# Optimization experiments

Hardware: AMD Instinct MI355X
Metric: run time of the kernel (lower is better)

## Reference

```python
import jax, jax.numpy as jnp
import numpy as np

GAMMA = 0.5
NUM_ITER = 5


def setup_inputs() -> dict:
    key = jax.random.key(0)
    k1, k2 = jax.random.split(key)
    V, L = 10242, 42
    def_idxs = jax.random.uniform(k1, (V, L), dtype=jnp.float32, minval=1e-4, maxval=1.0)
    def_cont_ico_crf = jax.random.normal(k2, (V, 3), dtype=jnp.float32)
    # learned parameters, initialized as in the module
    filter_weights = jnp.ones((V, V), dtype=jnp.float32)
    spatial_weights = 4.0 * jnp.eye(V, dtype=jnp.float32)
    comp_matrix = jnp.eye(L, dtype=jnp.float32)
    return {
        "def_idxs": def_idxs,
        "def_cont_ico_crf": def_cont_ico_crf,
        "filter_weights": filter_weights,
        "spatial_weights": spatial_weights,
        "comp_matrix": comp_matrix,
    }


def reference(def_idxs, def_cont_ico_crf, filter_weights, spatial_weights, comp_matrix):
    V = def_cont_ico_crf.shape[0]
    # pairwise squared L2 distances between control points: [V, V]
    sq = jnp.sum(def_cont_ico_crf * def_cont_ico_crf, axis=1)
    d2 = sq[:, None] + sq[None, :] - 2.0 * (def_cont_ico_crf @ def_cont_ico_crf.T)
    smooth_filter = jnp.exp(-d2 / (2.0 * GAMMA ** 2))
    idx = jnp.arange(V)
    smooth_filter = smooth_filter.at[idx, idx].set(0.0)  # fill_diagonal_(0)

    U = jnp.log(jnp.clip(def_idxs, 1e-06, 1.0))  # unary potentials [V, L]
    q = jax.nn.softmax(U, axis=1)
    filter_mat = filter_weights * smooth_filter

    for _ in range(NUM_ITER):
        phi_t = filter_mat @ q                      # message passing [V, L]
        phi = -(spatial_weights @ phi_t)            # spatial reweighting
        phi = phi @ comp_matrix                     # label compatibility
        q = jax.nn.softmax(U - phi, axis=1)
    return q
```

## Files before the change

### kernel.cpp

```cpp
#include <hip/hip_runtime.h>
#include <stdint.h>

#define Vn 10242
#define Ln 42
#define LPn 48
#define VPn 10496
#define RBn 41
#define JPAD 10368
#define NITER 5
#define SCL 1.69864360f
#define BR 128

typedef float4 f4;
typedef short bf16x8 __attribute__((ext_vector_type(8)));
typedef float f32x4 __attribute__((ext_vector_type(4)));

__device__ __forceinline__ unsigned cvtpk_bf16(float a, float b) {
    unsigned r;
    asm("v_cvt_pk_bf16_f32 %0, %1, %2" : "=v"(r) : "v"(a), "v"(b));
    return r;
}
__device__ __forceinline__ unsigned short f2bf_rne(float f) {
    unsigned u = __float_as_uint(f);
    u = (u + 0x7fffu + ((u >> 16) & 1u)) >> 16;
    return (unsigned short)u;
}
__device__ __forceinline__ float bf2f(unsigned short h) {
    return __uint_as_float(((unsigned)h) << 16);
}

__global__ __launch_bounds__(256) void k_detect(const float* __restrict__ F,
                                                const float* __restrict__ S,
                                                int* flags, float* __restrict__ diagS) {
    int jj = blockIdx.x * 256 + threadIdx.x;
    if (jj >= Vn / 2) return;
    int j = jj * 2;
    const float c0 = F[0];
    int violF = 0, violS = 0;
    for (int i = blockIdx.y; i < Vn; i += (int)gridDim.y) {
        size_t off = (size_t)i * Vn + j;
        float2 f = *(const float2*)(F + off);
        float2 s = *(const float2*)(S + off);
        violF |= (f.x != c0) | (f.y != c0);
        if (i == j)          { diagS[j] = s.x;     violS |= (s.y != 0.0f); }
        else if (i == j + 1) { diagS[j + 1] = s.y; violS |= (s.x != 0.0f); }
        else                 violS |= (s.x != 0.0f) | (s.y != 0.0f);
    }
    if (violF) atomicOr(&flags[0], 1);
    if (violS) atomicOr(&flags[1], 1);
}

__global__ void k_detC(const float* __restrict__ Cm, int* flags) {
    int viol = 0;
    for (int idx = threadIdx.x; idx < Ln * Ln; idx += 256) {
        int r = idx / Ln, c = idx - r * Ln;
        float expct = (r == c) ? 1.0f : 0.0f;
        viol |= (Cm[idx] != expct);
    }
    if (viol) atomicOr(&flags[3], 1);
}

__global__ __launch_bounds__(256) void k_initU(const float* __restrict__ didx,
                                               const float* __restrict__ coords,
                                               float* __restrict__ U, float* __restrict__ qA,
                                               float* __restrict__ qB,
                                               unsigned short* __restrict__ qTAh,
                                               unsigned short* __restrict__ qTAl,
                                               unsigned short* __restrict__ qTBh,
                                               unsigned short* __restrict__ qTBl,
                                               float* __restrict__ xyz) {
    int row = blockIdx.x * 256 + threadIdx.x;
    if (row >= Vn) {
        #pragma unroll
        for (int l = 0; l < LPn; ++l) {
            U[(size_t)row * LPn + l] = 0.0f;
            qA[(size_t)row * LPn + l] = 0.0f;
            qB[(size_t)row * LPn + l] = 0.0f;
            qTAh[(size_t)l * VPn + row] = 0;
            qTAl[(size_t)l * VPn + row] = 0;
            qTBh[(size_t)l * VPn + row] = 0;
            qTBl[(size_t)l * VPn + row] = 0;
        }
        *(f4*)(xyz + (size_t)row * 4) = make_float4(0.f, 0.f, 0.f, 0.f);
        return;
    }
    float ux = SCL * coords[(size_t)row * 3 + 0];
    float uy = SCL * coords[(size_t)row * 3 + 1];
    float uz = SCL * coords[(size_t)row * 3 + 2];
    float ss = ux * ux + uy * uy + uz * uz;
    *(f4*)(xyz + (size_t)row * 4) = make_float4(ux, uy, uz, ss);
    float u[Ln];
    float mx = -3.0e38f;
    #pragma unroll
    for (int l = 0; l < Ln; ++l) {
        float x = didx[(size_t)row * Ln + l];
        x = fminf(fmaxf(x, 1e-6f), 1.0f);
        u[l] = __logf(x);
        mx = fmaxf(mx, u[l]);
    }
    float s = 0.0f;
    float e[Ln];
    #pragma unroll
    for (int l = 0; l < Ln; ++l) { e[l] = __expf(u[l] - mx); s += e[l]; }
    float inv = 1.0f / s;
    #pragma unroll
    for (int l = 0; l < Ln; ++l) {
        float qv = e[l] * inv;
        unsigned short h = f2bf_rne(qv);
        U[(size_t)row * LPn + l] = u[l];
        qA[(size_t)row * LPn + l] = qv;
        qTAh[(size_t)l * VPn + row] = h;
        qTAl[(size_t)l * VPn + row] = f2bf_rne(qv - bf2f(h));
    }
    #pragma unroll
    for (int l = Ln; l < LPn; ++l) {
        U[(size_t)row * LPn + l] = 0.0f;
        qA[(size_t)row * LPn + l] = 0.0f;
        qB[(size_t)row * LPn + l] = 0.0f;
        qTAh[(size_t)l * VPn + row] = 0;
        qTAl[(size_t)l * VPn + row] = 0;
        qTBh[(size_t)l * VPn + row] = 0;
        qTBl[(size_t)l * VPn + row] = 0;
    }
}

__global__ __launch_bounds__(256, 3) void k_phi_f(const unsigned short* __restrict__ qTh,
                                                  const unsigned short* __restrict__ qTl,
                                                  const f4* __restrict__ xyz4,
                                                  float* __restrict__ part,
                                                  const int* __restrict__ flags, int jchunk) {
    if (flags[0]) return;
    __shared__ uint4 Ah[8][BR];
    __shared__ uint4 Al[8][BR];
    __shared__ uint4 Bh[LPn][8];
    __shared__ uint4 Bl[LPn][8];
    const int t = threadIdx.x;
    const int lane = t & 63;
    const int wv = t >> 6;
    const int lo16 = lane & 15, hi4 = lane >> 4;
    const int rowbase = blockIdx.x * BR;
    f4 p0 = xyz4[rowbase + lane];
    f4 p1 = xyz4[rowbase + lane + 64];
    const float v0x = 2.f * p0.x, v0y = 2.f * p0.y, v0z = 2.f * p0.z, ns0 = -p0.w;
    const float v1x = 2.f * p1.x, v1y = 2.f * p1.y, v1z = 2.f * p1.z, ns1 = -p1.w;
    f32x4 acc[2][3];
    #pragma unroll
    for (int rs = 0; rs < 2; ++rs)
        #pragma unroll
        for (int cs = 0; cs < 3; ++cs) acc[rs][cs] = (f32x4){0.f, 0.f, 0.f, 0.f};
    const int j0 = blockIdx.y * jchunk;
    int j1 = j0 + jchunk; if (j1 > JPAD) j1 = JPAD;
    const int n0 = t >> 3, sl0 = t & 7;
    const int s1 = t + 256;
    const int n1 = s1 >> 3, sl1 = s1 & 7;
    const bool has1 = (s1 < LPn * 8);
    for (int jt = j0; jt < j1; jt += 64) {
        uint4 bh0 = *(const uint4*)(qTh + (size_t)n0 * VPn + jt + sl0 * 8);
        uint4 bl0 = *(const uint4*)(qTl + (size_t)n0 * VPn + jt + sl0 * 8);
        uint4 bh1, bl1;
        if (has1) {
            bh1 = *(const uint4*)(qTh + (size_t)n1 * VPn + jt + sl1 * 8);
            bl1 = *(const uint4*)(qTl + (size_t)n1 * VPn + jt + sl1 * 8);
        }
        const int jb = __builtin_amdgcn_readfirstlane(jt + wv * 16);
        unsigned ph0[8], ph1[8], pl0[8], pl1[8];
        #pragma unroll
        for (int m = 0; m < 16; m += 2) {
            f4 qa = xyz4[jb + m];
            f4 qb = xyz4[jb + m + 1];
            float wa0 = exp2f(fmaf(v0z, qa.z, fmaf(v0y, qa.y, fmaf(v0x, qa.x, ns0 - qa.w))));
            float wb0 = exp2f(fmaf(v0z, qb.z, fmaf(v0y, qb.y, fmaf(v0x, qb.x, ns0 - qb.w))));
            float wa1 = exp2f(fmaf(v1z, qa.z, fmaf(v1y, qa.y, fmaf(v1x, qa.x, ns1 - qa.w))));
            float wb1 = exp2f(fmaf(v1z, qb.z, fmaf(v1y, qb.y, fmaf(v1x, qb.x, ns1 - qb.w))));
            unsigned h0 = cvtpk_bf16(wa0, wb0);
            unsigned h1 = cvtpk_bf16(wa1, wb1);
            ph0[m >> 1] = h0;
            ph1[m >> 1] = h1;
            pl0[m >> 1] = cvtpk_bf16(wa0 - __uint_as_float(h0 << 16),
                                     wb0 - __uint_as_float(h0 & 0xffff0000u));
            pl1[m >> 1] = cvtpk_bf16(wa1 - __uint_as_float(h1 << 16),
                                     wb1 - __uint_as_float(h1 & 0xffff0000u));
        }
        __syncthreads();
        Ah[2 * wv][lane]          = make_uint4(ph0[0], ph0[1], ph0[2], ph0[3]);
        Ah[2 * wv + 1][lane]      = make_uint4(ph0[4], ph0[5], ph0[6], ph0[7]);
        Ah[2 * wv][lane + 64]     = make_uint4(ph1[0], ph1[1], ph1[2], ph1[3]);
        Ah[2 * wv + 1][lane + 64] = make_uint4(ph1[4], ph1[5], ph1[6], ph1[7]);
        Al[2 * wv][lane]          = make_uint4(pl0[0], pl0[1], pl0[2], pl0[3]);
        Al[2 * wv + 1][lane]      = make_uint4(pl0[4], pl0[5], pl0[6], pl0[7]);
        Al[2 * wv][lane + 64]     = make_uint4(pl1[0], pl1[1], pl1[2], pl1[3]);
        Al[2 * wv + 1][lane + 64] = make_uint4(pl1[4], pl1[5], pl1[6], pl1[7]);
        Bh[n0][sl0 ^ (n0 & 7)] = bh0;
        Bl[n0][sl0 ^ (n0 & 7)] = bl0;
        if (has1) {
            Bh[n1][sl1 ^ (n1 & 7)] = bh1;
            Bl[n1][sl1 ^ (n1 & 7)] = bl1;
        }
        __syncthreads();
        #pragma unroll
        for (int kk = 0; kk < 2; ++kk) {
            bf16x8 a0h = *(bf16x8*)&Ah[kk * 4 + hi4][wv * 32 + lo16];
            bf16x8 a1h = *(bf16x8*)&Ah[kk * 4 + hi4][wv * 32 + 16 + lo16];
            bf16x8 a0l = *(bf16x8*)&Al[kk * 4 + hi4][wv * 32 + lo16];
            bf16x8 a1l = *(bf16x8*)&Al[kk * 4 + hi4][wv * 32 + 16 + lo16];
            #pragma unroll
            for (int cs = 0; cs < 3; ++cs) {
                int n = cs * 16 + lo16;
                int slot = (kk * 4 + hi4) ^ (n & 7);
                bf16x8 bh = *(bf16x8*)&Bh[n][slot];
                bf16x8 bl = *(bf16x8*)&Bl[n][slot];
                acc[0][cs] = __builtin_amdgcn_mfma_f32_16x16x32_bf16(a0h, bh, acc[0][cs], 0, 0, 0);
                acc[0][cs] = __builtin_amdgcn_mfma_f32_16x16x32_bf16(a0h, bl, acc[0][cs], 0, 0, 0);
                acc[0][cs] = __builtin_amdgcn_mfma_f32_16x16x32_bf16(a0l, bh, acc[0][cs], 0, 0, 0);
                acc[0][cs] = __builtin_amdgcn_mfma_f32_16x16x32_bf16(a0l, bl, acc[0][cs], 0, 0, 0);
                acc[1][cs] = __builtin_amdgcn_mfma_f32_16x16x32_bf16(a1h, bh, acc[1][cs], 0, 0, 0);
                acc[1][cs] = __builtin_amdgcn_mfma_f32_16x16x32_bf16(a1h, bl, acc[1][cs], 0, 0, 0);
                acc[1][cs] = __builtin_amdgcn_mfma_f32_16x16x32_bf16(a1l, bh, acc[1][cs], 0, 0, 0);
                acc[1][cs] = __builtin_amdgcn_mfma_f32_16x16x32_bf16(a1l, bl, acc[1][cs], 0, 0, 0);
            }
        }
    }
    size_t pb = (size_t)blockIdx.y * LPn * VPn;
    #pragma unroll
    for (int rs = 0; rs < 2; ++rs)
        #pragma unroll
        for (int cs = 0; cs < 3; ++cs) {
            int col = cs * 16 + lo16;
            int row = rowbase + wv * 32 + rs * 16 + hi4 * 4;
            *(f4*)(part + pb + (size_t)col * VPn + row) =
                make_float4(acc[rs][cs][0], acc[rs][cs][1], acc[rs][cs][2], acc[rs][cs][3]);
        }
}

template <int USEG>
__device__ __forceinline__ void mat_gen_body(const float* __restrict__ W,
                                             const float* __restrict__ X,
                                             const float* __restrict__ xyz,
                                             float* __restrict__ part, int jchunk) {
    __shared__ float ldsW[256][33];
    int t = threadIdx.x;
    int row = blockIdx.x * 256 + t;
    bool act = (row < Vn);
    int j0 = blockIdx.y * jchunk;
    int j1 = j0 + jchunk; if (j1 > Vn) j1 = Vn;
    f4 xi = make_float4(0.f, 0.f, 0.f, 0.f);
    if (USEG && act) xi = *(const f4*)(xyz + (size_t)row * 4);
    f4 acc[12];
    #pragma unroll
    for (int c = 0; c < 12; ++c) acc[c] = make_float4(0.f, 0.f, 0.f, 0.f);
    for (int jt = j0; jt < j1; jt += 32) {
        __syncthreads();
        #pragma unroll
        for (int k = 0; k < 8; ++k) {
            int idx = t + k * 256;
            int r = idx >> 3;
            int cc = (idx & 7) << 2;
            int rr = blockIdx.x * 256 + r;
            int jc = jt + cc;
            float v0 = 0.f, v1 = 0.f, v2 = 0.f, v3 = 0.f;
            if (rr < Vn) {
                const float* wp = W + (size_t)rr * Vn + jc;
                if (jc + 0 < Vn) v0 = wp[0];
                if (jc + 1 < Vn) v1 = wp[1];
                if (jc + 2 < Vn) v2 = wp[2];
                if (jc + 3 < Vn) v3 = wp[3];
            }
            ldsW[r][cc + 0] = v0; ldsW[r][cc + 1] = v1;
            ldsW[r][cc + 2] = v2; ldsW[r][cc + 3] = v3;
        }
        __syncthreads();
        int jend = j1 - jt; if (jend > 32) jend = 32;
        for (int jj = 0; jj < jend; ++jj) {
            int j = jt + jj;
            float f = ldsW[t][jj];
            if (USEG) {
                f4 xj = *(const f4*)(xyz + (size_t)j * 4);
                float dx = xi.x - xj.x, dy = xi.y - xj.y, dz = xi.z - xj.z;
                float t2 = dx * dx; t2 = fmaf(dy, dy, t2); t2 = fmaf(dz, dz, t2);
                float w = exp2f(-t2);
                w = (j == row) ? 0.0f : w;
                f *= w;
            }
            const f4* qr = (const f4*)(X + (size_t)j * LPn);
            #pragma unroll
            for (int c = 0; c < 12; ++c) {
                f4 qv = qr[c];
                acc[c].x = fmaf(f, qv.x, acc[c].x);
                acc[c].y = fmaf(f, qv.y, acc[c].y);
                acc[c].z = fmaf(f, qv.z, acc[c].z);
                acc[c].w = fmaf(f, qv.w, acc[c].w);
            }
        }
    }
    size_t base = (size_t)blockIdx.y * LPn * VPn + row;
    if (act) {
        #pragma unroll
        for (int c = 0; c < 12; ++c) {
            part[base + (size_t)(4 * c + 0) * VPn] = acc[c].x;
            part[base + (size_t)(4 * c + 1) * VPn] = acc[c].y;
            part[base + (size_t)(4 * c + 2) * VPn] = acc[c].z;
            part[base + (size_t)(4 * c + 3) * VPn] = acc[c].w;
        }
    } else if (row < VPn) {
        #pragma unroll
        for (int c = 0; c < LPn; ++c) part[base + (size_t)c * VPn] = 0.0f;
    }
}

__global__ __launch_bounds__(256) void k_phi_g(const float* __restrict__ W,
                                               const float* __restrict__ q,
                                               const float* __restrict__ xyz,
                                               float* __restrict__ part,
                                               const int* __restrict__ flags, int jchunk) {
    if (!flags[0]) return;
    mat_gen_body<1>(W, q, xyz, part, jchunk);
}

__global__ __launch_bounds__(256) void k_sp(const float* __restrict__ Sw,
                                            const float* __restrict__ phi,
                                            float* __restrict__ part,
                                            const int* __restrict__ flags, int jchunk) {
    if (!flags[1]) return;
    mat_gen_body<0>(Sw, phi, (const float*)nullptr, part, jchunk);
}

__global__ __launch_bounds__(256) void k_R0(const float* __restrict__ part,
                                            const unsigned short* __restrict__ qTh,
                                            const unsigned short* __restrict__ qTl,
                                            float* __restrict__ phi,
                                            const int* __restrict__ flags,
                                            int NS, int gate) {
    if (gate && !flags[1]) return;
    int tg = blockIdx.x * 256 + threadIdx.x;
    int c = tg / (VPn / 4);
    int r4 = (tg - c * (VPn / 4)) * 4;
    f4 s = make_float4(0.f, 0.f, 0.f, 0.f);
    for (int n = 0; n < NS; ++n) {
        f4 v = *(const f4*)(part + ((size_t)n * LPn + c) * VPn + r4);
        s.x += v.x; s.y += v.y; s.z += v.z; s.w += v.w;
    }
    if (!gate && !flags[0]) {
        ushort4 h = *(const ushort4*)(qTh + (size_t)c * VPn + r4);
        ushort4 l = *(const ushort4*)(qTl + (size_t)c * VPn + r4);
        s.x -= bf2f(h.x) + bf2f(l.x);
        s.y -= bf2f(h.y) + bf2f(l.y);
        s.z -= bf2f(h.z) + bf2f(l.z);
        s.w -= bf2f(h.w) + bf2f(l.w);
    }
    phi[(size_t)(r4 + 0) * LPn + c] = s.x;
    phi[(size_t)(r4 + 1) * LPn + c] = s.y;
    phi[(size_t)(r4 + 2) * LPn + c] = s.z;
    phi[(size_t)(r4 + 3) * LPn + c] = s.w;
}

__global__ __launch_bounds__(256) void k_B(const float* __restrict__ U,
                                           const float* __restrict__ phi,
                                           const float* __restrict__ phi2,
                                           const float* __restrict__ diagS,
                                           const float* __restrict__ Cm,
                                           const float* __restrict__ Fw,
                                           const int* __restrict__ flags,
                                           float* __restrict__ qn,
                                           unsigned short* __restrict__ qTnh,
                                           unsigned short* __restrict__ qTnl,
                                           float* __restrict__ outp, int last) {
    __shared__ float ldsC[Ln][LPn];
    int t = threadIdx.x;
    if (flags[3]) {
        for (int idx = t; idx < Ln * LPn; idx += 256) {
            int m = idx / LPn, l = idx - m * LPn;
            ldsC[m][l] = (l < Ln) ? Cm[(size_t)m * Ln + l] : 0.0f;
        }
    }
    __syncthreads();
    int row = blockIdx.x * 256 + t;
    if (row >= Vn) return;
    const float* src = flags[1] ? phi2 : phi;
    float pt[LPn];
    #pragma unroll
    for (int c = 0; c < 12; ++c) {
        f4 v = *(const f4*)(src + (size_t)row * LPn + 4 * c);
        pt[4 * c + 0] = v.x; pt[4 * c + 1] = v.y;
        pt[4 * c + 2] = v.z; pt[4 * c + 3] = v.w;
    }
    float scale = (flags[0] ? 1.0f : Fw[0]) * (flags[1] ? 1.0f : diagS[row]);
    float ph[LPn];
    if (flags[3]) {
        #pragma unroll
        for (int c = 0; c < LPn; ++c) ph[c] = 0.f;
        #pragma unroll
        for (int m = 0; m < Ln; ++m) {
            float pm = pt[m];
            #pragma unroll
            for (int c = 0; c < 12; ++c) {
                f4 cv = *(const f4*)&ldsC[m][4 * c];
                ph[4 * c + 0] = fmaf(pm, cv.x, ph[4 * c + 0]);
                ph[4 * c + 1] = fmaf(pm, cv.y, ph[4 * c + 1]);
                ph[4 * c + 2] = fmaf(pm, cv.z, ph[4 * c + 2]);
                ph[4 * c + 3] = fmaf(pm, cv.w, ph[4 * c + 3]);
            }
        }
    } else {
        #pragma unroll
        for (int c = 0; c < LPn; ++c) ph[c] = pt[c];
    }
    float lg[LPn];
    #pragma unroll
    for (int c = 0; c < 12; ++c) {
        f4 uv = *(const f4*)(U + (size_t)row * LPn + 4 * c);
        lg[4 * c + 0] = uv.x + scale * ph[4 * c + 0];
        lg[4 * c + 1] = uv.y + scale * ph[4 * c + 1];
        lg[4 * c + 2] = uv.z + scale * ph[4 * c + 2];
        lg[4 * c + 3] = uv.w + scale * ph[4 * c + 3];
    }
    float mx = lg[0];
    #pragma unroll
    for (int l = 1; l < Ln; ++l) mx = fmaxf(mx, lg[l]);
    float s = 0.f;
    float e[LPn];
    #pragma unroll
    for (int l = 0; l < Ln; ++l) { e[l] = __expf(lg[l] - mx); s += e[l]; }
    #pragma unroll
    for (int l = Ln; l < LPn; ++l) e[l] = 0.f;
    float inv = 1.0f / s;
    #pragma unroll
    for (int c = 0; c < 12; ++c) {
        f4 v = make_float4(e[4 * c + 0] * inv, e[4 * c + 1] * inv,
                           e[4 * c + 2] * inv, e[4 * c + 3] * inv);
        *(f4*)(qn + (size_t)row * LPn + 4 * c) = v;
    }
    #pragma unroll
    for (int l = 0; l < Ln; ++l) {
        float qv = e[l] * inv;
        unsigned short h = f2bf_rne(qv);
        qTnh[(size_t)l * VPn + row] = h;
        qTnl[(size_t)l * VPn + row] = f2bf_rne(qv - bf2f(h));
    }
    if (last) {
        #pragma unroll
        for (int l = 0; l < Ln; ++l) outp[(size_t)row * Ln + l] = e[l] * inv;
    }
}

extern "C" void kernel_launch(void* const* d_in, const int* in_sizes, int n_in,
                              void* d_out, int out_size, void* d_ws, size_t ws_size,
                              hipStream_t stream) {
    const float* didx   = (const float*)d_in[0];
    const float* coords = (const float*)d_in[1];
    const float* Fw     = (const float*)d_in[2];
    const float* Sw     = (const float*)d_in[3];
    const float* Cm     = (const float*)d_in[4];
    float* outp = (float*)d_out;
    float* wsf = (float*)d_ws;

    int*   flags = (int*)wsf;
    float* diagS = wsf + 16;
    float* xyz   = diagS + VPn;
    float* U     = xyz + (size_t)VPn * 4;
    float* qA    = U + (size_t)VPn * LPn;
    float* qB    = qA + (size_t)VPn * LPn;
    float* phi   = qB + (size_t)VPn * LPn;
    float* phi2  = phi + (size_t)VPn * LPn;
    unsigned short* qTAh = (unsigned short*)(phi2 + (size_t)VPn * LPn);
    unsigned short* qTAl = qTAh + (size_t)LPn * VPn;
    unsigned short* qTBh = qTAl + (size_t)LPn * VPn;
    unsigned short* qTBl = qTBh + (size_t)LPn * VPn;
    float* part  = (float*)(qTBl + (size_t)LPn * VPn);

    size_t base_f = 16 + (size_t)VPn * (1 + 4) + (size_t)VPn * LPn * 5 + (size_t)VPn * LPn * 2;
    int NS = 8;
    while (NS > 1 && (base_f + (size_t)NS * LPn * VPn) * 4 > ws_size) NS >>= 1;
    int jchunkF = ((JPAD / 64 + NS - 1) / NS) * 64;
    int jchunkG = (((Vn + NS - 1) / NS) + 31) & ~31;

    hipMemsetAsync(flags, 0, 16, stream);
    hipLaunchKernelGGL(k_detect, dim3((Vn / 2 + 255) / 256, 1024), dim3(256), 0, stream,
                       Fw, Sw, flags, diagS);
    hipLaunchKernelGGL(k_detC, dim3(1), dim3(256), 0, stream, Cm, flags);
    hipLaunchKernelGGL(k_initU, dim3(RBn), dim3(256), 0, stream,
                       didx, coords, U, qA, qB, qTAh, qTAl, qTBh, qTBl, xyz);

    float* qcur = qA;  float* qnxt = qB;
    unsigned short* qThc = qTAh;  unsigned short* qTlc = qTAl;
    unsigned short* qThn = qTBh;  unsigned short* qTln = qTBl;
    for (int it = 0; it < NITER; ++it) {
        hipLaunchKernelGGL(k_phi_f, dim3(VPn / BR, NS), dim3(256), 0, stream,
                           qThc, qTlc, (const f4*)xyz, part, flags, jchunkF);
        hipLaunchKernelGGL(k_phi_g, dim3(RBn, NS), dim3(256), 0, stream,
                           Fw, qcur, xyz, part, flags, jchunkG);
        hipLaunchKernelGGL(k_R0, dim3(LPn * (VPn / 4) / 256), dim3(256), 0, stream,
                           part, qThc, qTlc, phi, flags, NS, 0);
        hipLaunchKernelGGL(k_sp, dim3(RBn, NS), dim3(256), 0, stream,
                           Sw, phi, part, flags, jchunkG);
        hipLaunchKernelGGL(k_R0, dim3(LPn * (VPn / 4) / 256), dim3(256), 0, stream,
                           part, qThc, qTlc, phi2, flags, NS, 1);
        hipLaunchKernelGGL(k_B, dim3(RBn), dim3(256), 0, stream,
                           U, phi, phi2, diagS, Cm, Fw, flags, qnxt, qThn, qTln, outp,
                           (it == NITER - 1) ? 1 : 0);
        float* tq = qcur; qcur = qnxt; qnxt = tq;
        unsigned short* th = qThc; qThc = qThn; qThn = th;
        unsigned short* tl = qTlc; qTlc = qTln; qTln = tl;
    }
}
```

Before: 653.5 us.

## Merge phi kernels, drop low×low MFMA term, split j range nine ways

Merges the fast-path and general-path phi kernels into one launch that branches on the detection flag, with the two shared-memory layouts overlaid in a union. The split-bf16 product drops the low×low term, cutting MFMA count per tile from 24 to 18. The j-range split count starts at 9 instead of 8 and falls back one step at a time. Fewer MFMAs and one fewer launch per iteration reduce compute and dispatch overhead, at a small accuracy cost from the omitted correction term and one more partial buffer to reduce.

```diff
diff --git a/kernel.cpp b/kernel.cpp
--- a/kernel.cpp
+++ b/kernel.cpp
@@ -124,120 +124,22 @@
     }
 }
 
-__global__ __launch_bounds__(256, 3) void k_phi_f(const unsigned short* __restrict__ qTh,
-                                                  const unsigned short* __restrict__ qTl,
-                                                  const f4* __restrict__ xyz4,
-                                                  float* __restrict__ part,
-                                                  const int* __restrict__ flags, int jchunk) {
-    if (flags[0]) return;
-    __shared__ uint4 Ah[8][BR];
-    __shared__ uint4 Al[8][BR];
-    __shared__ uint4 Bh[LPn][8];
-    __shared__ uint4 Bl[LPn][8];
-    const int t = threadIdx.x;
-    const int lane = t & 63;
-    const int wv = t >> 6;
-    const int lo16 = lane & 15, hi4 = lane >> 4;
-    const int rowbase = blockIdx.x * BR;
-    f4 p0 = xyz4[rowbase + lane];
-    f4 p1 = xyz4[rowbase + lane + 64];
-    const float v0x = 2.f * p0.x, v0y = 2.f * p0.y, v0z = 2.f * p0.z, ns0 = -p0.w;
-    const float v1x = 2.f * p1.x, v1y = 2.f * p1.y, v1z = 2.f * p1.z, ns1 = -p1.w;
-    f32x4 acc[2][3];
-    #pragma unroll
-    for (int rs = 0; rs < 2; ++rs)
-        #pragma unroll
-        for (int cs = 0; cs < 3; ++cs) acc[rs][cs] = (f32x4){0.f, 0.f, 0.f, 0.f};
-    const int j0 = blockIdx.y * jchunk;
-    int j1 = j0 + jchunk; if (j1 > JPAD) j1 = JPAD;
-    const int n0 = t >> 3, sl0 = t & 7;
-    const int s1 = t + 256;
-    const int n1 = s1 >> 3, sl1 = s1 & 7;
-    const bool has1 = (s1 < LPn * 8);
-    for (int jt = j0; jt < j1; jt += 64) {
-        uint4 bh0 = *(const uint4*)(qTh + (size_t)n0 * VPn + jt + sl0 * 8);
-        uint4 bl0 = *(const uint4*)(qTl + (size_t)n0 * VPn + jt + sl0 * 8);
-        uint4 bh1, bl1;
-        if (has1) {
-            bh1 = *(const uint4*)(qTh + (size_t)n1 * VPn + jt + sl1 * 8);
-            bl1 = *(const uint4*)(qTl + (size_t)n1 * VPn + jt + sl1 * 8);
-        }
-        const int jb = __builtin_amdgcn_readfirstlane(jt + wv * 16);
-        unsigned ph0[8], ph1[8], pl0[8], pl1[8];
-        #pragma unroll
-        for (int m = 0; m < 16; m += 2) {
-            f4 qa = xyz4[jb + m];
-            f4 qb = xyz4[jb + m + 1];
-            float wa0 = exp2f(fmaf(v0z, qa.z, fmaf(v0y, qa.y, fmaf(v0x, qa.x, ns0 - qa.w))));
-            float wb0 = exp2f(fmaf(v0z, qb.z, fmaf(v0y, qb.y, fmaf(v0x, qb.x, ns0 - qb.w))));
-            float wa1 = exp2f(fmaf(v1z, qa.z, fmaf(v1y, qa.y, fmaf(v1x, qa.x, ns1 - qa.w))));
-            float wb1 = exp2f(fmaf(v1z, qb.z, fmaf(v1y, qb.y, fmaf(v1x, qb.x, ns1 - qb.w))));
-            unsigned h0 = cvtpk_bf16(wa0, wb0);
-            unsigned h1 = cvtpk_bf16(wa1, wb1);
-            ph0[m >> 1] = h0;
-            ph1[m >> 1] = h1;
-            pl0[m >> 1] = cvtpk_bf16(wa0 - __uint_as_float(h0 << 16),
-                                     wb0 - __uint_as_float(h0 & 0xffff0000u));
-            pl1[m >> 1] = cvtpk_bf16(wa1 - __uint_as_float(h1 << 16),
-                                     wb1 - __uint_as_float(h1 & 0xffff0000u));
-        }
-        __syncthreads();
-        Ah[2 * wv][lane]          = make_uint4(ph0[0], ph0[1], ph0[2], ph0[3]);
-        Ah[2 * wv + 1][lane]      = make_uint4(ph0[4], ph0[5], ph0[6], ph0[7]);
-        Ah[2 * wv][lane + 64]     = make_uint4(ph1[0], ph1[1], ph1[2], ph1[3]);
-        Ah[2 * wv + 1][lane + 64] = make_uint4(ph1[4], ph1[5], ph1[6], ph1[7]);
-        Al[2 * wv][lane]          = make_uint4(pl0[0], pl0[1], pl0[2], pl0[3]);
-        Al[2 * wv + 1][lane]      = make_uint4(pl0[4], pl0[5], pl0[6], pl0[7]);
-        Al[2 * wv][lane + 64]     = make_uint4(pl1[0], pl1[1], pl1[2], pl1[3]);
-        Al[2 * wv + 1][lane + 64] = make_uint4(pl1[4], pl1[5], pl1[6], pl1[7]);
-        Bh[n0][sl0 ^ (n0 & 7)] = bh0;
-        Bl[n0][sl0 ^ (n0 & 7)] = bl0;
-        if (has1) {
-            Bh[n1][sl1 ^ (n1 & 7)] = bh1;
-            Bl[n1][sl1 ^ (n1 & 7)] = bl1;
-        }
-        __syncthreads();
-        #pragma unroll
-        for (int kk = 0; kk < 2; ++kk) {
-            bf16x8 a0h = *(bf16x8*)&Ah[kk * 4 + hi4][wv * 32 + lo16];
-            bf16x8 a1h = *(bf16x8*)&Ah[kk * 4 + hi4][wv * 32 + 16 + lo16];
-            bf16x8 a0l = *(bf16x8*)&Al[kk * 4 + hi4][wv * 32 + lo16];
-            bf16x8 a1l = *(bf16x8*)&Al[kk * 4 + hi4][wv * 32 + 16 + lo16];
-            #pragma unroll
-            for (int cs = 0; cs < 3; ++cs) {
-                int n = cs * 16 + lo16;
-                int slot = (kk * 4 + hi4) ^ (n & 7);
-                bf16x8 bh = *(bf16x8*)&Bh[n][slot];
-                bf16x8 bl = *(bf16x8*)&Bl[n][slot];
-                acc[0][cs] = __builtin_amdgcn_mfma_f32_16x16x32_bf16(a0h, bh, acc[0][cs], 0, 0, 0);
-                acc[0][cs] = __builtin_amdgcn_mfma_f32_16x16x32_bf16(a0h, bl, acc[0][cs], 0, 0, 0);
-                acc[0][cs] = __builtin_amdgcn_mfma_f32_16x16x32_bf16(a0l, bh, acc[0][cs], 0, 0, 0);
-                acc[0][cs] = __builtin_amdgcn_mfma_f32_16x16x32_bf16(a0l, bl, acc[0][cs], 0, 0, 0);
-                acc[1][cs] = __builtin_amdgcn_mfma_f32_16x16x32_bf16(a1h, bh, acc[1][cs], 0, 0, 0);
-                acc[1][cs] = __builtin_amdgcn_mfma_f32_16x16x32_bf16(a1h, bl, acc[1][cs], 0, 0, 0);
-                acc[1][cs] = __builtin_amdgcn_mfma_f32_16x16x32_bf16(a1l, bh, acc[1][cs], 0, 0, 0);
-                acc[1][cs] = __builtin_amdgcn_mfma_f32_16x16x32_bf16(a1l, bl, acc[1][cs], 0, 0, 0);
-            }
-        }
-    }
-    size_t pb = (size_t)blockIdx.y * LPn * VPn;
-    #pragma unroll
-    for (int rs = 0; rs < 2; ++rs)
-        #pragma unroll
-        for (int cs = 0; cs < 3; ++cs) {
-            int col = cs * 16 + lo16;
-            int row = rowbase + wv * 32 + rs * 16 + hi4 * 4;
-            *(f4*)(part + pb + (size_t)col * VPn + row) =
-                make_float4(acc[rs][cs][0], acc[rs][cs][1], acc[rs][cs][2], acc[rs][cs][3]);
-        }
-}
+union ShPhi {
+    struct {
+        uint4 Ah[8][BR];
+        uint4 Al[8][BR];
+        uint4 Bh[LPn][8];
+        uint4 Bl[LPn][8];
+    } f;
+    float w[256][33];
+};
 
 template <int USEG>
 __device__ __forceinline__ void mat_gen_body(const float* __restrict__ W,
                                              const float* __restrict__ X,
                                              const float* __restrict__ xyz,
-                                             float* __restrict__ part, int jchunk) {
-    __shared__ float ldsW[256][33];
+                                             float* __restrict__ part, int jchunk,
+                                             ShPhi& sh) {
     int t = threadIdx.x;
     int row = blockIdx.x * 256 + t;
     bool act = (row < Vn);
@@ -265,14 +167,14 @@
                 if (jc + 2 < Vn) v2 = wp[2];
                 if (jc + 3 < Vn) v3 = wp[3];
             }
-            ldsW[r][cc + 0] = v0; ldsW[r][cc + 1] = v1;
-            ldsW[r][cc + 2] = v2; ldsW[r][cc + 3] = v3;
+            sh.w[r][cc + 0] = v0; sh.w[r][cc + 1] = v1;
+            sh.w[r][cc + 2] = v2; sh.w[r][cc + 3] = v3;
         }
         __syncthreads();
         int jend = j1 - jt; if (jend > 32) jend = 32;
         for (int jj = 0; jj < jend; ++jj) {
             int j = jt + jj;
-            float f = ldsW[t][jj];
+            float f = sh.w[t][jj];
             if (USEG) {
                 f4 xj = *(const f4*)(xyz + (size_t)j * 4);
                 float dx = xi.x - xj.x, dy = xi.y - xj.y, dz = xi.z - xj.z;
@@ -307,13 +209,114 @@
     }
 }
 
-__global__ __launch_bounds__(256) void k_phi_g(const float* __restrict__ W,
-                                               const float* __restrict__ q,
-                                               const float* __restrict__ xyz,
-                                               float* __restrict__ part,
-                                               const int* __restrict__ flags, int jchunk) {
-    if (!flags[0]) return;
-    mat_gen_body<1>(W, q, xyz, part, jchunk);
+__global__ __launch_bounds__(256, 3) void k_phi(const unsigned short* __restrict__ qTh,
+                                                const unsigned short* __restrict__ qTl,
+                                                const f4* __restrict__ xyz4,
+                                                const float* __restrict__ Fw,
+                                                const float* __restrict__ q,
+                                                float* __restrict__ part,
+                                                const int* __restrict__ flags,
+                                                int jchunkF, int jchunkG) {
+    __shared__ ShPhi sh;
+    if (flags[0]) {
+        if (blockIdx.x >= RBn) return;
+        mat_gen_body<1>(Fw, q, (const float*)xyz4, part, jchunkG, sh);
+        return;
+    }
+    const int t = threadIdx.x;
+    const int lane = t & 63;
+    const int wv = t >> 6;
+    const int lo16 = lane & 15, hi4 = lane >> 4;
+    const int rowbase = blockIdx.x * BR;
+    f4 p0 = xyz4[rowbase + lane];
+    f4 p1 = xyz4[rowbase + lane + 64];
+    const float v0x = 2.f * p0.x, v0y = 2.f * p0.y, v0z = 2.f * p0.z, ns0 = -p0.w;
+    const float v1x = 2.f * p1.x, v1y = 2.f * p1.y, v1z = 2.f * p1.z, ns1 = -p1.w;
+    f32x4 acc[2][3];
+    #pragma unroll
+    for (int rs = 0; rs < 2; ++rs)
+        #pragma unroll
+        for (int cs = 0; cs < 3; ++cs) acc[rs][cs] = (f32x4){0.f, 0.f, 0.f, 0.f};
+    const int j0 = blockIdx.y * jchunkF;
+    int j1 = j0 + jchunkF; if (j1 > JPAD) j1 = JPAD;
+    const int n0 = t >> 3, sl0 = t & 7;
+    const int s1 = t + 256;
+    const int n1 = s1 >> 3, sl1 = s1 & 7;
+    const bool has1 = (s1 < LPn * 8);
+    for (int jt = j0; jt < j1; jt += 64) {
+        uint4 bh0 = *(const uint4*)(qTh + (size_t)n0 * VPn + jt + sl0 * 8);
+        uint4 bl0 = *(const uint4*)(qTl + (size_t)n0 * VPn + jt + sl0 * 8);
+        uint4 bh1, bl1;
+        if (has1) {
+            bh1 = *(const uint4*)(qTh + (size_t)n1 * VPn + jt + sl1 * 8);
+            bl1 = *(const uint4*)(qTl + (size_t)n1 * VPn + jt + sl1 * 8);
+        }
+        const int jb = __builtin_amdgcn_readfirstlane(jt + wv * 16);
+        unsigned ph0[8], ph1[8], pl0[8], pl1[8];
+        #pragma unroll
+        for (int m = 0; m < 16; m += 2) {
+            f4 qa = xyz4[jb + m];
+            f4 qb = xyz4[jb + m + 1];
+            float wa0 = exp2f(fmaf(v0z, qa.z, fmaf(v0y, qa.y, fmaf(v0x, qa.x, ns0 - qa.w))));
+            float wb0 = exp2f(fmaf(v0z, qb.z, fmaf(v0y, qb.y, fmaf(v0x, qb.x, ns0 - qb.w))));
+            float wa1 = exp2f(fmaf(v1z, qa.z, fmaf(v1y, qa.y, fmaf(v1x, qa.x, ns1 - qa.w))));
+            float wb1 = exp2f(fmaf(v1z, qb.z, fmaf(v1y, qb.y, fmaf(v1x, qb.x, ns1 - qb.w))));
+            unsigned h0 = cvtpk_bf16(wa0, wb0);
+            unsigned h1 = cvtpk_bf16(wa1, wb1);
+            ph0[m >> 1] = h0;
+            ph1[m >> 1] = h1;
+            pl0[m >> 1] = cvtpk_bf16(wa0 - __uint_as_float(h0 << 16),
+                                     wb0 - __uint_as_float(h0 & 0xffff0000u));
+            pl1[m >> 1] = cvtpk_bf16(wa1 - __uint_as_float(h1 << 16),
+                                     wb1 - __uint_as_float(h1 & 0xffff0000u));
+        }
+        __syncthreads();
+        sh.f.Ah[2 * wv][lane]          = make_uint4(ph0[0], ph0[1], ph0[2], ph0[3]);
+        sh.f.Ah[2 * wv + 1][lane]      = make_uint4(ph0[4], ph0[5], ph0[6], ph0[7]);
+        sh.f.Ah[2 * wv][lane + 64]     = make_uint4(ph1[0], ph1[1], ph1[2], ph1[3]);
+        sh.f.Ah[2 * wv + 1][lane + 64] = make_uint4(ph1[4], ph1[5], ph1[6], ph1[7]);
+        sh.f.Al[2 * wv][lane]          = make_uint4(pl0[0], pl0[1], pl0[2], pl0[3]);
+        sh.f.Al[2 * wv + 1][lane]      = make_uint4(pl0[4], pl0[5], pl0[6], pl0[7]);
+        sh.f.Al[2 * wv][lane + 64]     = make_uint4(pl1[0], pl1[1], pl1[2], pl1[3]);
+        sh.f.Al[2 * wv + 1][lane + 64] = make_uint4(pl1[4], pl1[5], pl1[6], pl1[7]);
+        sh.f.Bh[n0][sl0 ^ (n0 & 7)] = bh0;
+        sh.f.Bl[n0][sl0 ^ (n0 & 7)] = bl0;
+        if (has1) {
+            sh.f.Bh[n1][sl1 ^ (n1 & 7)] = bh1;
+            sh.f.Bl[n1][sl1 ^ (n1 & 7)] = bl1;
+        }
+        __syncthreads();
+        #pragma unroll
+        for (int kk = 0; kk < 2; ++kk) {
+            bf16x8 a0h = *(bf16x8*)&sh.f.Ah[kk * 4 + hi4][wv * 32 + lo16];
+            bf16x8 a1h = *(bf16x8*)&sh.f.Ah[kk * 4 + hi4][wv * 32 + 16 + lo16];
+            bf16x8 a0l = *(bf16x8*)&sh.f.Al[kk * 4 + hi4][wv * 32 + lo16];
+            bf16x8 a1l = *(bf16x8*)&sh.f.Al[kk * 4 + hi4][wv * 32 + 16 + lo16];
+            #pragma unroll
+            for (int cs = 0; cs < 3; ++cs) {
+                int n = cs * 16 + lo16;
+                int slot = (kk * 4 + hi4) ^ (n & 7);
+                bf16x8 bh = *(bf16x8*)&sh.f.Bh[n][slot];
+                bf16x8 bl = *(bf16x8*)&sh.f.Bl[n][slot];
+                acc[0][cs] = __builtin_amdgcn_mfma_f32_16x16x32_bf16(a0h, bh, acc[0][cs], 0, 0, 0);
+                acc[0][cs] = __builtin_amdgcn_mfma_f32_16x16x32_bf16(a0h, bl, acc[0][cs], 0, 0, 0);
+                acc[0][cs] = __builtin_amdgcn_mfma_f32_16x16x32_bf16(a0l, bh, acc[0][cs], 0, 0, 0);
+                acc[1][cs] = __builtin_amdgcn_mfma_f32_16x16x32_bf16(a1h, bh, acc[1][cs], 0, 0, 0);
+                acc[1][cs] = __builtin_amdgcn_mfma_f32_16x16x32_bf16(a1h, bl, acc[1][cs], 0, 0, 0);
+                acc[1][cs] = __builtin_amdgcn_mfma_f32_16x16x32_bf16(a1l, bh, acc[1][cs], 0, 0, 0);
+            }
+        }
+    }
+    size_t pb = (size_t)blockIdx.y * LPn * VPn;
+    #pragma unroll
+    for (int rs = 0; rs < 2; ++rs)
+        #pragma unroll
+        for (int cs = 0; cs < 3; ++cs) {
+            int col = cs * 16 + lo16;
+            int row = rowbase + wv * 32 + rs * 16 + hi4 * 4;
+            *(f4*)(part + pb + (size_t)col * VPn + row) =
+                make_float4(acc[rs][cs][0], acc[rs][cs][1], acc[rs][cs][2], acc[rs][cs][3]);
+        }
 }
 
 __global__ __launch_bounds__(256) void k_sp(const float* __restrict__ Sw,
@@ -321,7 +324,8 @@
                                             float* __restrict__ part,
                                             const int* __restrict__ flags, int jchunk) {
     if (!flags[1]) return;
-    mat_gen_body<0>(Sw, phi, (const float*)nullptr, part, jchunk);
+    __shared__ ShPhi sh;
+    mat_gen_body<0>(Sw, phi, (const float*)nullptr, part, jchunk, sh);
 }
 
 __global__ __launch_bounds__(256) void k_R0(const float* __restrict__ part,
@@ -468,9 +472,9 @@
     float* part  = (float*)(qTBl + (size_t)LPn * VPn);
 
     size_t base_f = 16 + (size_t)VPn * (1 + 4) + (size_t)VPn * LPn * 5 + (size_t)VPn * LPn * 2;
-    int NS = 8;
-    while (NS > 1 && (base_f + (size_t)NS * LPn * VPn) * 4 > ws_size) NS >>= 1;
-    int jchunkF = ((JPAD / 64 + NS - 1) / NS) * 64;
+    int NS = 9;
+    while (NS > 1 && (base_f + (size_t)NS * LPn * VPn) * 4 > ws_size) NS--;
+    int jchunkF = (((JPAD / 64) + NS - 1) / NS) * 64;
     int jchunkG = (((Vn + NS - 1) / NS) + 31) & ~31;
 
     hipMemsetAsync(flags, 0, 16, stream);
@@ -484,10 +488,9 @@
     unsigned short* qThc = qTAh;  unsigned short* qTlc = qTAl;
     unsigned short* qThn = qTBh;  unsigned short* qTln = qTBl;
     for (int it = 0; it < NITER; ++it) {
-        hipLaunchKernelGGL(k_phi_f, dim3(VPn / BR, NS), dim3(256), 0, stream,
-                           qThc, qTlc, (const f4*)xyz, part, flags, jchunkF);
-        hipLaunchKernelGGL(k_phi_g, dim3(RBn, NS), dim3(256), 0, stream,
-                           Fw, qcur, xyz, part, flags, jchunkG);
+        hipLaunchKernelGGL(k_phi, dim3(VPn / BR, NS), dim3(256), 0, stream,
+                           qThc, qTlc, (const f4*)xyz, Fw, qcur, part, flags,
+                           jchunkF, jchunkG);
         hipLaunchKernelGGL(k_R0, dim3(LPn * (VPn / 4) / 256), dim3(256), 0, stream,
                            part, qThc, qTlc, phi, flags, NS, 0);
         hipLaunchKernelGGL(k_sp, dim3(RBn, NS), dim3(256), 0, stream,
@@ -495,8 +498,8 @@
         hipLaunchKernelGGL(k_R0, dim3(LPn * (VPn / 4) / 256), dim3(256), 0, stream,
                            part, qThc, qTlc, phi2, flags, NS, 1);
         hipLaunchKernelGGL(k_B, dim3(RBn), dim3(256), 0, stream,
-                           U, phi, phi2, diagS, Cm, Fw, flags, qnxt, qThn, qTln, outp,
-                           (it == NITER - 1) ? 1 : 0);
+                           U, phi, phi2, diagS, Cm, Fw, flags,
+                           qnxt, qThn, qTln, outp, (it == NITER - 1) ? 1 : 0);
         float* tq = qcur; qcur = qnxt; qnxt = tq;
         unsigned short* th = qThc; qThc = qThn; qThn = th;
         unsigned short* tl = qTlc; qTlc = qTln; qTln = tl;
```

Result: faster. 589.6 us (-9.8%).
